# Kernel tuning notes

Measured on AMD Instinct MI355X. Metric: run time of the kernel, lower is better.

Reference implementation:

```python
import jax, jax.numpy as jnp
import numpy as np

T_STEPS = 4
TAU = 2.0
EPS = 1e-5
NUM_HEADS = 8
SCALE = 0.125  # hardcoded self.scale in the torch module
SG_ALPHA = 4.0  # spikingjelly default sigmoid surrogate alpha


@jax.custom_vjp
def heaviside(x):
    return (x >= 0.0).astype(x.dtype)

def _hv_fwd(x):
    return heaviside(x), x

def _hv_bwd(x, g):
    s = jax.nn.sigmoid(SG_ALPHA * x)
    return (g * SG_ALPHA * s * (1.0 - s),)

heaviside.defvjp(_hv_fwd, _hv_bwd)


def lif(x_seq, v_th):
    # MultiStepLIFNode: v += (x - v)/tau; spike = H(v - v_th); hard reset to 0 (detached).
    def step(v, x):
        v = v + (x - v) / TAU
        s = heaviside(v - v_th)
        v = v * (1.0 - jax.lax.stop_gradient(s))
        return v, s
    _, out = jax.lax.scan(step, jnp.zeros_like(x_seq[0]), x_seq)
    return out


def bn(x, g, b):
    # BatchNorm1d training-mode stats over (batch, length) per channel; x: (TB, C, N)
    m = jnp.mean(x, axis=(0, 2), keepdims=True)
    var = jnp.mean((x - m) ** 2, axis=(0, 2), keepdims=True)
    return g[None, :, None] * (x - m) * jax.lax.rsqrt(var + EPS) + b[None, :, None]


def _branch(x, w, b, g, beta):
    # linear over channel dim + BN + LIF, then split heads -> (T,B,H,N,d)
    T, B, C, N = x.shape
    y = jnp.einsum('oc,tbcn->tbon', w, x) + b[None, None, :, None]
    y = bn(y.reshape(T * B, C, N), g, beta).reshape(T, B, C, N)
    y = lif(y, 1.0)
    d = C // NUM_HEADS
    return y.transpose(0, 1, 3, 2).reshape(T, B, N, NUM_HEADS, d).transpose(0, 1, 3, 2, 4)


def setup_inputs() -> dict:
    key = jax.random.key(0)
    ks = jax.random.split(key, 6)
    B, C, N = 8, 512, 1024
    bound = float(np.sqrt(6.0 / (3 * C + C)))  # xavier_uniform for (3C, C)
    return {
        'q': jax.random.normal(ks[0], (B, C, N), jnp.float32),
        'k': jax.random.normal(ks[1], (B, C, N), jnp.float32),
        'v': jax.random.normal(ks[2], (B, C, N), jnp.float32),
        'in_proj_w': jax.random.uniform(ks[3], (3 * C, C), jnp.float32, -bound, bound),
        'in_proj_b': jnp.zeros((3 * C,), jnp.float32),
        'q_gamma': jnp.ones((C,), jnp.float32),
        'q_beta': jnp.zeros((C,), jnp.float32),
        'k_gamma': jnp.ones((C,), jnp.float32),
        'k_beta': jnp.zeros((C,), jnp.float32),
        'v_gamma': jnp.ones((C,), jnp.float32),
        'v_beta': jnp.zeros((C,), jnp.float32),
        'proj_w': jax.random.normal(ks[4], (C, C), jnp.float32) * (1.0 / np.sqrt(C)),
        'proj_b': jnp.zeros((C,), jnp.float32),
        'p_gamma': jnp.ones((C,), jnp.float32),
        'p_beta': jnp.zeros((C,), jnp.float32),
    }


def reference(q, k, v, in_proj_w, in_proj_b, q_gamma, q_beta, k_gamma, k_beta,
              v_gamma, v_beta, proj_w, proj_b, p_gamma, p_beta):
    B, C, N = q.shape
    qs = jnp.broadcast_to(q[None], (T_STEPS, B, C, N))
    ks_ = jnp.broadcast_to(k[None], (T_STEPS, B, C, N))
    vs = jnp.broadcast_to(v[None], (T_STEPS, B, C, N))

    qh = _branch(qs, in_proj_w[:C], in_proj_b[:C], q_gamma, q_beta)        # (T,B,H,N,d)
    kh = _branch(ks_, in_proj_w[C:2 * C], in_proj_b[C:2 * C], k_gamma, k_beta)
    vh = _branch(vs, in_proj_w[2 * C:], in_proj_b[2 * C:], v_gamma, v_beta)

    # linear attention: (k^T v) then q @ (k^T v)
    ktv = jnp.einsum('tbhnd,tbhne->tbhde', kh, vh)            # (T,B,H,d,d)
    att = jnp.einsum('tbhnd,tbhde->tbhne', qh, ktv) * SCALE   # (T,B,H,N,d)

    x = att.transpose(0, 1, 2, 4, 3).reshape(T_STEPS, B, C, N)
    x = lif(x, 0.5)  # attn_lif with v_threshold=0.5

    z = jnp.einsum('oc,tbcn->tbon', proj_w, x) + proj_b[None, None, :, None]  # 1x1 conv
    z = bn(z.reshape(T_STEPS * B, C, N), p_gamma, p_beta).reshape(T_STEPS, B, C, N)
    return lif(z, 1.0)
```

## Files before the change

### kernel.cpp

```cpp
#include <hip/hip_runtime.h>

#define C    512
#define NDIM 1024
#define BDIM 8
#define TDIM 4
#define HDIM 8
#define CN   (C*NDIM)
#define BCN  (BDIM*CN)

typedef unsigned short u16;
typedef unsigned int   u32;
typedef unsigned long long u64;
typedef __attribute__((ext_vector_type(8))) short bf8v;
typedef __attribute__((ext_vector_type(8))) _Float16 h8v;
typedef __attribute__((ext_vector_type(4))) float f4v;
typedef __attribute__((ext_vector_type(2))) float f2v;

__device__ __forceinline__ u16 f2bf(float f) {
    u32 u = __float_as_uint(f);
    u32 r = u + 0x7FFFu + ((u >> 16) & 1u);
    return (u16)(r >> 16);
}
__device__ __forceinline__ float bf2f(u16 h) { return __uint_as_float((u32)h << 16); }

#if defined(__has_builtin)
#if __has_builtin(__builtin_amdgcn_global_load_lds)
#define HAS_GLL 1
#endif
#if __has_builtin(__builtin_elementwise_fma)
#define HAS_EFMA 1
#endif
#endif
#ifdef HAS_GLL
#define GLD(gp, lp) __builtin_amdgcn_global_load_lds( \
    (const __attribute__((address_space(1))) u32*)(gp), \
    (__attribute__((address_space(3))) u32*)(lp), 16, 0, 0)
#else
#define GLD(gp, lp) (*(uint4*)(lp) = *(const uint4*)(const void*)(gp))
#endif

__device__ __forceinline__ f2v pkfma(f2v a, f2v b, f2v c) {
#ifdef HAS_EFMA
    return __builtin_elementwise_fma(a, b, c);
#else
    f2v r; r.x = fmaf(a.x, b.x, c.x); r.y = fmaf(a.y, b.y, c.y); return r;
#endif
}

__global__ __launch_bounds__(256) void gemm_in3_k(
    const float* __restrict__ W, const float* __restrict__ bias,
    const float* __restrict__ Xq, const float* __restrict__ Xk,
    const float* __restrict__ Xv, float* __restrict__ Y3)
{
    __shared__ float As[16][132];
    __shared__ float Bs[16][132];
    const int tid = threadIdx.x;
    const int bz = blockIdx.z;
    const int br = bz >> 3, b = bz & 7;
    const int m0 = blockIdx.y * 128;
    const int n0 = blockIdx.x * 128;
    const float* Xb = (br == 0 ? Xq : (br == 1 ? Xk : Xv)) + (size_t)b * CN;
    const int rowOff = br * 512;

    const int ra = tid >> 2, ka = (tid & 3) * 4;
    const int kb = tid >> 5, nb = (tid & 31) * 4;
    const int tx = tid & 15, ty = tid >> 4;

    const float* pA0 = &W[(size_t)(rowOff + m0 + ra) * 512 + ka];
    const float* pA1 = &W[(size_t)(rowOff + m0 + 64 + ra) * 512 + ka];
    const float* pB0 = &Xb[(size_t)kb * NDIM + n0 + nb];
    const float* pB1 = &Xb[(size_t)(kb + 8) * NDIM + n0 + nb];

    f2v acc[2][2][4][2];
    #pragma unroll
    for (int mq = 0; mq < 2; mq++)
        #pragma unroll
        for (int nq = 0; nq < 2; nq++)
            #pragma unroll
            for (int i = 0; i < 4; i++)
                #pragma unroll
                for (int jp = 0; jp < 2; jp++) acc[mq][nq][i][jp] = (f2v){0.f, 0.f};

    float4 a0 = *(const float4*)pA0;
    float4 a1 = *(const float4*)pA1;
    float4 b0 = *(const float4*)pB0;
    float4 b1 = *(const float4*)pB1;

    for (int k0 = 0; k0 < 512; k0 += 16) {
        __syncthreads();
        As[ka + 0][ra] = a0.x; As[ka + 1][ra] = a0.y;
        As[ka + 2][ra] = a0.z; As[ka + 3][ra] = a0.w;
        As[ka + 0][64 + ra] = a1.x; As[ka + 1][64 + ra] = a1.y;
        As[ka + 2][64 + ra] = a1.z; As[ka + 3][64 + ra] = a1.w;
        *(float4*)&Bs[kb][nb]     = b0;
        *(float4*)&Bs[kb + 8][nb] = b1;
        __syncthreads();
        if (k0 < 496) {
            a0 = *(const float4*)(pA0 + k0 + 16);
            a1 = *(const float4*)(pA1 + k0 + 16);
            b0 = *(const float4*)(pB0 + (size_t)(k0 + 16) * NDIM);
            b1 = *(const float4*)(pB1 + (size_t)(k0 + 16) * NDIM);
        }
        #pragma unroll
        for (int k = 0; k < 16; k++) {
            float av[2][4];
            f2v bv[2][2];
            *(float4*)av[0] = *(const float4*)&As[k][ty * 4];
            *(float4*)av[1] = *(const float4*)&As[k][64 + ty * 4];
            float4 bq0 = *(const float4*)&Bs[k][tx * 4];
            float4 bq1 = *(const float4*)&Bs[k][64 + tx * 4];
            bv[0][0] = (f2v){bq0.x, bq0.y}; bv[0][1] = (f2v){bq0.z, bq0.w};
            bv[1][0] = (f2v){bq1.x, bq1.y}; bv[1][1] = (f2v){bq1.z, bq1.w};
            #pragma unroll
            for (int mq = 0; mq < 2; mq++)
                #pragma unroll
                for (int i = 0; i < 4; i++) {
                    const f2v a2 = (f2v){av[mq][i], av[mq][i]};
                    #pragma unroll
                    for (int nq = 0; nq < 2; nq++)
                        #pragma unroll
                        for (int jp = 0; jp < 2; jp++)
                            acc[mq][nq][i][jp] = pkfma(a2, bv[nq][jp], acc[mq][nq][i][jp]);
                }
        }
    }
    #pragma unroll
    for (int mq = 0; mq < 2; mq++)
        #pragma unroll
        for (int i = 0; i < 4; i++) {
            const int mrow = mq * 64 + ty * 4 + i;
            float bsv = bias[rowOff + m0 + mrow];
            float* yr = Y3 + (size_t)bz * CN + (size_t)(m0 + mrow) * NDIM + n0;
            #pragma unroll
            for (int nq = 0; nq < 2; nq++) {
                float4 o4 = make_float4(acc[mq][nq][i][0].x + bsv, acc[mq][nq][i][0].y + bsv,
                                        acc[mq][nq][i][1].x + bsv, acc[mq][nq][i][1].y + bsv);
                *(float4*)&yr[nq * 64 + tx * 4] = o4;
            }
        }
}

__global__ __launch_bounds__(256) void chan_stats2_k(
    const float* __restrict__ X3, float* __restrict__ mean3,
    float* __restrict__ rstd3, int outer)
{
    __shared__ float red[256];
    __shared__ float m_sh;
    const int gb = blockIdx.x;
    const int o = gb & (C - 1);
    const float* X = X3 + (size_t)(gb >> 9) * BCN;
    const int tid = threadIdx.x;
    const int total = outer * NDIM;
    float s = 0.f;
    for (int i = tid; i < total; i += 256) {
        int ou = i >> 10, n = i & 1023;
        s += X[(size_t)(ou * C + o) * NDIM + n];
    }
    red[tid] = s; __syncthreads();
    for (int off = 128; off > 0; off >>= 1) {
        if (tid < off) red[tid] += red[tid + off];
        __syncthreads();
    }
    if (tid == 0) { float m = red[0] / (float)total; mean3[gb] = m; m_sh = m; }
    __syncthreads();
    const float m = m_sh;
    float s2 = 0.f;
    for (int i = tid; i < total; i += 256) {
        int ou = i >> 10, n = i & 1023;
        float d = X[(size_t)(ou * C + o) * NDIM + n] - m;
        s2 += d * d;
    }
    red[tid] = s2; __syncthreads();
    for (int off = 128; off > 0; off >>= 1) {
        if (tid < off) red[tid] += red[tid + off];
        __syncthreads();
    }
    if (tid == 0) rstd3[gb] = 1.f / sqrtf(red[0] / (float)total + 1e-5f);
}

__global__ __launch_bounds__(256) void spikes_k(
    const float* __restrict__ Y3, const float* __restrict__ mean3,
    const float* __restrict__ rstd3,
    const float* __restrict__ qg, const float* __restrict__ qb,
    const float* __restrict__ kg, const float* __restrict__ kbt,
    const float* __restrict__ vg, const float* __restrict__ vbt,
    const float* __restrict__ PW,
    u64* __restrict__ qm, u64* __restrict__ kbits, u64* __restrict__ vbits,
    u16* __restrict__ Ps)
{
    __shared__ unsigned char tile[64][68];
    const int tid = threadIdx.x;
    const int bid = blockIdx.x;
    if (bid < 1024) {
        const int b = bid >> 7, h = (bid >> 4) & 7, nt = bid & 15;
        const int c_l = tid >> 2, sg = (tid & 3) * 16;
        const int o = h * 64 + c_l;
        const float m = mean3[o], rs = rstd3[o], g = qg[o], bt = qb[o];
        const float* Yr = Y3 + ((size_t)b * C + o) * NDIM + nt * 64 + sg;
        #pragma unroll
        for (int j = 0; j < 4; j++) {
            float4 y4 = *(const float4*)&Yr[j * 4];
            float ys[4] = {y4.x, y4.y, y4.z, y4.w};
            #pragma unroll
            for (int e = 0; e < 4; e++) {
                float x = g * (ys[e] - m);
                x = x * rs + bt;
                float v = 0.f; unsigned bits = 0;
                #pragma unroll
                for (int t = 0; t < 4; t++) {
                    v += (x - v) * 0.5f;
                    if (v - 1.0f >= 0.f) { bits |= (1u << t); v = 0.f; }
                }
                tile[c_l][sg + j * 4 + e] = (unsigned char)bits;
            }
        }
        __syncthreads();
        const int lane = tid & 63, wv = tid >> 6;
        #pragma unroll
        for (int i = 0; i < 16; i++) {
            const int nl = wv * 16 + i;
            unsigned s = tile[lane][nl];
            #pragma unroll
            for (int t = 0; t < 4; t++) {
                u64 mk = __ballot((s >> t) & 1);
                if (lane == t)
                    qm[(size_t)((t * BDIM + b) * HDIM + h) * NDIM + nt * 64 + nl] = mk;
            }
        }
    } else if (bid < 3072) {
        const int r = bid - 1024;
        const int br = r >> 10;
        const int rr = r & 1023;
        const int b = rr >> 7, ct = (rr >> 4) & 7, nt = rr & 15;
        const float* Yb = Y3 + (size_t)(br + 1) * BCN + (size_t)b * CN;
        const float* mean = mean3 + (br + 1) * C;
        const float* rstd = rstd3 + (br + 1) * C;
        const float* gam = br == 0 ? kg : vg;
        const float* bet = br == 0 ? kbt : vbt;
        u64* bits = br == 0 ? kbits : vbits;
        const int lane = tid & 63, wv = tid >> 6;
        #pragma unroll
        for (int i = 0; i < 16; i++) {
            const int o = ct * 64 + wv * 16 + i;
            const float m = mean[o], rs = rstd[o], g = gam[o], bt = bet[o];
            float y = Yb[(size_t)o * NDIM + nt * 64 + lane];
            float x = g * (y - m);
            x = x * rs + bt;
            float v = 0.f; unsigned sb = 0;
            #pragma unroll
            for (int t = 0; t < 4; t++) {
                v += (x - v) * 0.5f;
                if (v - 1.0f >= 0.f) { sb |= (1u << t); v = 0.f; }
            }
            #pragma unroll
            for (int t = 0; t < 4; t++) {
                u64 mk = __ballot((sb >> t) & 1);
                if (lane == t)
                    bits[((size_t)(t * BDIM + b) * C + o) * 16 + nt] = mk;
            }
        }
    } else {
        const int idx = (bid - 3072) * 256 + tid;
        float x = PW[idx];
        u16 h1 = f2bf(x); float r1 = x - bf2f(h1);
        u16 h2 = f2bf(r1); float r2 = r1 - bf2f(h2);
        u16 h3 = f2bf(r2);
        Ps[idx] = h1; Ps[idx + 262144] = h2; Ps[idx + 2 * 262144] = h3;
    }
}

__global__ __launch_bounds__(256) void ktvT_k(
    const u64* __restrict__ kb, const u64* __restrict__ vb,
    _Float16* __restrict__ ktvT)
{
    __shared__ u64 kst[64][17];
    __shared__ u64 vst[64][17];
    const int tid = threadIdx.x;
    const int g = blockIdx.x;
    const int h = g & 7, b = (g >> 3) & 7, t = g >> 6;
    const size_t base = ((size_t)(t * BDIM + b) * C + h * 64) * 16;
    {
        int r = tid >> 2, w0 = (tid & 3) * 4;
        #pragma unroll
        for (int j = 0; j < 4; j++) {
            kst[r][w0 + j] = kb[base + r * 16 + w0 + j];
            vst[r][w0 + j] = vb[base + r * 16 + w0 + j];
        }
    }
    __syncthreads();
    const int e = tid >> 2, dd0 = (tid & 3) * 16;
    u64 vr[16];
    #pragma unroll
    for (int w = 0; w < 16; w++) vr[w] = vst[e][w];
    #pragma unroll
    for (int i = 0; i < 16; i++) {
        int dd = dd0 + i;
        int s = 0;
        #pragma unroll
        for (int w = 0; w < 16; w++) s += __popcll(kst[dd][w] & vr[w]);
        ktvT[(size_t)(g * 64 + e) * 64 + dd] = (_Float16)s;
    }
}

__global__ __launch_bounds__(256) void att_mfma_k(
    const _Float16* __restrict__ ktvT, const u64* __restrict__ qm,
    unsigned char* __restrict__ spkT)
{
    const int tid = threadIdx.x;
    const int w = tid >> 6, lane = tid & 63;
    const int ln = lane & 15, q = lane >> 4;
    const int bh = blockIdx.x; const int h = bh & 7, b = bh >> 3;
    const int n0 = blockIdx.y * 64 + w * 16;

    float v[4][4];
    u32 bits[4][4];
    #pragma unroll
    for (int et = 0; et < 4; et++)
        #pragma unroll
        for (int r = 0; r < 4; r++) { v[et][r] = 0.f; bits[et][r] = 0u; }

    #pragma unroll
    for (int t = 0; t < 4; t++) {
        const size_t gq = (size_t)(t * BDIM + b) * HDIM + h;
        const u64 qw = qm[gq * NDIM + n0 + ln];
        union { u16 s[8]; h8v v8; } a0u, a1u;
        #pragma unroll
        for (int j = 0; j < 8; j++) {
            a0u.s[j] = (u16)(((qw >> (q * 8 + j)) & 1ull) ? 0x3C00u : 0u);
            a1u.s[j] = (u16)(((qw >> (32 + q * 8 + j)) & 1ull) ? 0x3C00u : 0u);
        }
        const _Float16* kbp = ktvT + gq * 4096;
        f4v acc[4];
        #pragma unroll
        for (int et = 0; et < 4; et++) acc[et] = (f4v){0.f, 0.f, 0.f, 0.f};
        #pragma unroll
        for (int et = 0; et < 4; et++) {
            h8v b0 = *(const h8v*)(kbp + (et * 16 + ln) * 64 + q * 8);
            h8v b1 = *(const h8v*)(kbp + (et * 16 + ln) * 64 + 32 + q * 8);
            acc[et] = __builtin_amdgcn_mfma_f32_16x16x32_f16(a0u.v8, b0, acc[et], 0, 0, 0);
            acc[et] = __builtin_amdgcn_mfma_f32_16x16x32_f16(a1u.v8, b1, acc[et], 0, 0, 0);
        }
        #pragma unroll
        for (int et = 0; et < 4; et++)
            #pragma unroll
            for (int r = 0; r < 4; r++) {
                float x = acc[et][r] * 0.125f;
                float vv = v[et][r];
                vv += (x - vv) * 0.5f;
                if (vv - 0.5f >= 0.f) { bits[et][r] |= (1u << t); vv = 0.f; }
                v[et][r] = vv;
            }
    }
    #pragma unroll
    for (int et = 0; et < 4; et++)
        #pragma unroll
        for (int r = 0; r < 4; r++)
            spkT[((size_t)b * 1024 + n0 + q * 4 + r) * 512 + h * 64 + et * 16 + ln] =
                (unsigned char)bits[et][r];
}

__global__ __launch_bounds__(256, 2) void gemm_proj_mfma(
    const u16* __restrict__ Ps, const unsigned char* __restrict__ spkT,
    float* __restrict__ Z)
{
    __shared__ __align__(16) u16 Ab[2][12288];
    __shared__ __align__(16) u16 Bb[2][4096];
    const int tid = threadIdx.x;
    const int zb = blockIdx.z, t = zb >> 3, bb = zb & 7;
    const int m0 = blockIdx.y * 128, n0 = blockIdx.x * 128;

    u32 aoff[2][3];
    int lofs[2];
    #pragma unroll
    for (int r = 0; r < 2; r++) {
        const int cid = tid + (r << 8);
        const int mm = cid & 15, kg = (cid >> 4) & 3, mt = cid >> 6;
        lofs[r] = cid * 8;
        #pragma unroll
        for (int s = 0; s < 3; s++)
            aoff[r][s] = (u32)s * 262144u + (u32)(m0 + mt * 16 + mm) * 512u + kg * 8;
    }
    auto stageA = [&](int ki2, int p2) {
        const u32 kk = (u32)ki2 << 5;
        #pragma unroll
        for (int r = 0; r < 2; r++)
            #pragma unroll
            for (int s = 0; s < 3; s++)
                GLD(Ps + aoff[r][s] + kk, &Ab[p2][s * 4096 + lofs[r]]);
    };
    const int nn = tid & 15, ntl = (tid >> 4) & 7, seg = tid >> 7;
    const u32 srcB = ((u32)bb * 1024u + (u32)(n0 + ntl * 16 + nn)) * 512u + seg * 16;
    const int ldsB0 = (ntl * 64 + seg * 32 + nn) * 8;
    auto convB = [&](uint4 braw, int p2) {
        u32 bs[4] = {braw.x, braw.y, braw.z, braw.w};
        u32 wreg[8];
        #pragma unroll
        for (int qq = 0; qq < 4; qq++) {
            u32 vv = bs[qq] >> t;
            wreg[qq * 2 + 0] = ((vv & 1u) ? 0x3F80u : 0u) | ((vv & 0x100u) ? 0x3F800000u : 0u);
            wreg[qq * 2 + 1] = (((vv >> 16) & 1u) ? 0x3F80u : 0u) | ((vv & 0x1000000u) ? 0x3F800000u : 0u);
        }
        *(uint4*)&Bb[p2][ldsB0]       = make_uint4(wreg[0], wreg[1], wreg[2], wreg[3]);
        *(uint4*)&Bb[p2][ldsB0 + 128] = make_uint4(wreg[4], wreg[5], wreg[6], wreg[7]);
    };

    const int lane = tid & 63, wv = tid >> 6;
    const int wm = wv >> 1, wn = wv & 1;
    const int q = lane >> 4, ln = lane & 15;
    int afo[4], bfo[4];
    #pragma unroll
    for (int i = 0; i < 4; i++) {
        afo[i] = ((wm * 4 + i) * 64 + q * 16 + ln) * 8;
        bfo[i] = ((wn * 4 + i) * 64 + q * 16 + ln) * 8;
    }

    f4v acc[4][4];
    #pragma unroll
    for (int i = 0; i < 4; i++)
        #pragma unroll
        for (int j = 0; j < 4; j++) acc[i][j] = (f4v){0.f, 0.f, 0.f, 0.f};

    stageA(0, 0);
    convB(*(const uint4*)&spkT[srcB], 0);
    uint4 braw;
    for (int ki = 0; ki < 16; ki++) {
        const int p = ki & 1;
        __syncthreads();
        if (ki < 15) {
            stageA(ki + 1, p ^ 1);
            braw = *(const uint4*)&spkT[srcB + ((u32)(ki + 1) << 5)];
        }
        bf8v bf[4];
        #pragma unroll
        for (int j = 0; j < 4; j++) bf[j] = *(const bf8v*)&Bb[p][bfo[j]];
        #pragma unroll
        for (int sa = 0; sa < 3; sa++) {
            bf8v af[4];
            #pragma unroll
            for (int i = 0; i < 4; i++) af[i] = *(const bf8v*)&Ab[p][sa * 4096 + afo[i]];
            #pragma unroll
            for (int i = 0; i < 4; i++)
                #pragma unroll
                for (int j = 0; j < 4; j++)
                    acc[i][j] = __builtin_amdgcn_mfma_f32_16x16x32_bf16(af[i], bf[j], acc[i][j], 0, 0, 0);
        }
        if (ki < 15) convB(braw, p ^ 1);
    }
    float* Zb = Z + (size_t)zb * CN;
    #pragma unroll
    for (int i = 0; i < 4; i++) {
        const int row = m0 + (wm * 4 + i) * 16 + q * 4;
        #pragma unroll
        for (int g = 0; g < 4; g++) {
            float* zr = Zb + (size_t)(row + g) * 1024 + n0 + ln;
            #pragma unroll
            for (int j = 0; j < 4; j++)
                zr[(wn * 4 + j) * 16] = acc[i][j][g];
        }
    }
}

__global__ __launch_bounds__(256) void final_bn_lif_k(
    float* __restrict__ Z, const float* __restrict__ mean,
    const float* __restrict__ rstd, const float* __restrict__ gamma,
    const float* __restrict__ beta)
{
    const int idx = blockIdx.x * 256 + threadIdx.x;
    const int o = (idx >> 10) & (C - 1);
    const float m = mean[o], rs = rstd[o], g = gamma[o], bt = beta[o];
    float v = 0.f;
    float outs[4];
    #pragma unroll
    for (int t = 0; t < 4; t++) {
        float z = Z[(size_t)t * BCN + idx];
        float x = g * (z - m);
        x = x * rs + bt;
        v += (x - v) * 0.5f;
        float s = (v - 1.0f >= 0.f) ? 1.f : 0.f;
        v *= (1.f - s);
        outs[t] = s;
    }
    #pragma unroll
    for (int t = 0; t < 4; t++) Z[(size_t)t * BCN + idx] = outs[t];
}

extern "C" void kernel_launch(void* const* d_in, const int* in_sizes, int n_in,
                              void* d_out, int out_size, void* d_ws, size_t ws_size,
                              hipStream_t stream)
{
    const float* q     = (const float*)d_in[0];
    const float* k     = (const float*)d_in[1];
    const float* v     = (const float*)d_in[2];
    const float* W     = (const float*)d_in[3];
    const float* Wb    = (const float*)d_in[4];
    const float* qg    = (const float*)d_in[5];
    const float* qb    = (const float*)d_in[6];
    const float* kg    = (const float*)d_in[7];
    const float* kbt   = (const float*)d_in[8];
    const float* vg    = (const float*)d_in[9];
    const float* vbt   = (const float*)d_in[10];
    const float* pw    = (const float*)d_in[11];
    const float* pg    = (const float*)d_in[13];
    const float* pbeta = (const float*)d_in[14];

    char* p = (char*)d_ws;
    u64* qmv = (u64*)p;                     p += (size_t)TDIM * BDIM * HDIM * NDIM * 8;
    u64* kbits = (u64*)p;                   p += (size_t)TDIM * BDIM * C * 16 * 8;
    u64* vbits = (u64*)p;                   p += (size_t)TDIM * BDIM * C * 16 * 8;
    u16* Ps = (u16*)p;                      p += (size_t)3 * 262144 * 2;
    unsigned char* spkT = (unsigned char*)p; p += (size_t)BCN;
    _Float16* ktvT = (_Float16*)p;          p += (size_t)TDIM * BDIM * HDIM * 64 * 64 * 2;
    float* mean3 = (float*)p;               p += 8192;
    float* rstd3 = (float*)p;               p += 8192;

    float* Y3 = (float*)d_out;
    float* outF = (float*)d_out;

    gemm_in3_k<<<dim3(8, 4, 24), 256, 0, stream>>>(W, Wb, q, k, v, Y3);
    chan_stats2_k<<<3 * C, 256, 0, stream>>>(Y3, mean3, rstd3, BDIM);
    spikes_k<<<4096, 256, 0, stream>>>(Y3, mean3, rstd3, qg, qb, kg, kbt, vg, vbt,
                                       pw, qmv, kbits, vbits, Ps);
    ktvT_k<<<256, 256, 0, stream>>>(kbits, vbits, ktvT);
    att_mfma_k<<<dim3(64, 16), 256, 0, stream>>>(ktvT, qmv, spkT);
    gemm_proj_mfma<<<dim3(8, 4, 32), 256, 0, stream>>>(Ps, spkT, outF);
    chan_stats2_k<<<C, 256, 0, stream>>>(outF, mean3, rstd3, TDIM * BDIM);
    final_bn_lif_k<<<BCN / 256, 256, 0, stream>>>(outF, mean3, rstd3, pg, pbeta);
}
```

Measured before the change: 518.9 us.

## Read GEMM B operand directly from global and double-buffer A in LDS

```diff
diff --git a/kernel.cpp b/kernel.cpp
--- a/kernel.cpp
+++ b/kernel.cpp
@@ -52,8 +52,7 @@
     const float* __restrict__ Xq, const float* __restrict__ Xk,
     const float* __restrict__ Xv, float* __restrict__ Y3)
 {
-    __shared__ float As[16][132];
-    __shared__ float Bs[16][132];
+    __shared__ float As[2][16][132];
     const int tid = threadIdx.x;
     const int bz = blockIdx.z;
     const int br = bz >> 3, b = bz & 7;
@@ -63,13 +62,12 @@
     const int rowOff = br * 512;
 
     const int ra = tid >> 2, ka = (tid & 3) * 4;
-    const int kb = tid >> 5, nb = (tid & 31) * 4;
     const int tx = tid & 15, ty = tid >> 4;
 
     const float* pA0 = &W[(size_t)(rowOff + m0 + ra) * 512 + ka];
     const float* pA1 = &W[(size_t)(rowOff + m0 + 64 + ra) * 512 + ka];
-    const float* pB0 = &Xb[(size_t)kb * NDIM + n0 + nb];
-    const float* pB1 = &Xb[(size_t)(kb + 8) * NDIM + n0 + nb];
+    const float* pBlo = &Xb[n0 + tx * 4];
+    const float* pBhi = &Xb[n0 + 64 + tx * 4];
 
     f2v acc[2][2][4][2];
     #pragma unroll
@@ -81,34 +79,32 @@
                 #pragma unroll
                 for (int jp = 0; jp < 2; jp++) acc[mq][nq][i][jp] = (f2v){0.f, 0.f};
 
-    float4 a0 = *(const float4*)pA0;
-    float4 a1 = *(const float4*)pA1;
-    float4 b0 = *(const float4*)pB0;
-    float4 b1 = *(const float4*)pB1;
+    {
+        float4 a0 = *(const float4*)pA0;
+        float4 a1 = *(const float4*)pA1;
+        As[0][ka + 0][ra] = a0.x; As[0][ka + 1][ra] = a0.y;
+        As[0][ka + 2][ra] = a0.z; As[0][ka + 3][ra] = a0.w;
+        As[0][ka + 0][64 + ra] = a1.x; As[0][ka + 1][64 + ra] = a1.y;
+        As[0][ka + 2][64 + ra] = a1.z; As[0][ka + 3][64 + ra] = a1.w;
+    }
+    __syncthreads();
 
     for (int k0 = 0; k0 < 512; k0 += 16) {
-        __syncthreads();
-        As[ka + 0][ra] = a0.x; As[ka + 1][ra] = a0.y;
-        As[ka + 2][ra] = a0.z; As[ka + 3][ra] = a0.w;
-        As[ka + 0][64 + ra] = a1.x; As[ka + 1][64 + ra] = a1.y;
-        As[ka + 2][64 + ra] = a1.z; As[ka + 3][64 + ra] = a1.w;
-        *(float4*)&Bs[kb][nb]     = b0;
-        *(float4*)&Bs[kb + 8][nb] = b1;
-        __syncthreads();
-        if (k0 < 496) {
-            a0 = *(const float4*)(pA0 + k0 + 16);
-            a1 = *(const float4*)(pA1 + k0 + 16);
-            b0 = *(const float4*)(pB0 + (size_t)(k0 + 16) * NDIM);
-            b1 = *(const float4*)(pB1 + (size_t)(k0 + 16) * NDIM);
+        const int p = (k0 >> 4) & 1;
+        const bool more = (k0 < 496);
+        float4 na0, na1;
+        if (more) {
+            na0 = *(const float4*)(pA0 + k0 + 16);
+            na1 = *(const float4*)(pA1 + k0 + 16);
         }
         #pragma unroll
         for (int k = 0; k < 16; k++) {
             float av[2][4];
             f2v bv[2][2];
-            *(float4*)av[0] = *(const float4*)&As[k][ty * 4];
-            *(float4*)av[1] = *(const float4*)&As[k][64 + ty * 4];
-            float4 bq0 = *(const float4*)&Bs[k][tx * 4];
-            float4 bq1 = *(const float4*)&Bs[k][64 + tx * 4];
+            *(float4*)av[0] = *(const float4*)&As[p][k][ty * 4];
+            *(float4*)av[1] = *(const float4*)&As[p][k][64 + ty * 4];
+            float4 bq0 = *(const float4*)(pBlo + (size_t)(k0 + k) * NDIM);
+            float4 bq1 = *(const float4*)(pBhi + (size_t)(k0 + k) * NDIM);
             bv[0][0] = (f2v){bq0.x, bq0.y}; bv[0][1] = (f2v){bq0.z, bq0.w};
             bv[1][0] = (f2v){bq1.x, bq1.y}; bv[1][1] = (f2v){bq1.z, bq1.w};
             #pragma unroll
@@ -123,6 +119,13 @@
                             acc[mq][nq][i][jp] = pkfma(a2, bv[nq][jp], acc[mq][nq][i][jp]);
                 }
         }
+        if (more) {
+            As[p ^ 1][ka + 0][ra] = na0.x; As[p ^ 1][ka + 1][ra] = na0.y;
+            As[p ^ 1][ka + 2][ra] = na0.z; As[p ^ 1][ka + 3][ra] = na0.w;
+            As[p ^ 1][ka + 0][64 + ra] = na1.x; As[p ^ 1][ka + 1][64 + ra] = na1.y;
+            As[p ^ 1][ka + 2][64 + ra] = na1.z; As[p ^ 1][ka + 3][64 + ra] = na1.w;
+        }
+        __syncthreads();
     }
     #pragma unroll
     for (int mq = 0; mq < 2; mq++)
```

New measurement: 603.0 us. 1.16x slower.
